# Kernel tuning notes

Hardware: AMD Instinct MI355X
Metric: run time of the kernel (lower is better)

The kernel has to match this reference:

```python
import jax, jax.numpy as jnp
import numpy as np

NUM_HEADS = 8
WINDOW = 7      # window_size -> K = 49 neighbors
DILATION = 1


def setup_inputs() -> dict:
    key = jax.random.key(0)
    k1, k2, k3 = jax.random.split(key, 3)
    shape = (4, 256, 48, 48)  # [B, C, H, W], C = num_heads * d_head
    return {
        "q": jax.random.normal(k1, shape, jnp.float32),
        "k": jax.random.normal(k2, shape, jnp.float32),
        "v": jax.random.normal(k3, shape, jnp.float32),
    }


def _neighbors(x, window, dilation):
    # x: [B, h, d, H, W] -> [B, h, K, d, H, W] via pad-and-slice shifts
    B, h, d, H, W = x.shape
    r = window // 2
    p = r * dilation
    xp = jnp.pad(x, ((0, 0), (0, 0), (0, 0), (p, p), (p, p)))
    offs = [(i - r) * dilation for i in range(window)]
    sl = [xp[:, :, :, p + dy:p + dy + H, p + dx:p + dx + W]
          for dy in offs for dx in offs]
    return jnp.stack(sl, axis=2)


def _valid_mask(H, W, window, dilation):
    # [K, H, W] boolean: True where the shifted neighbor is in-bounds
    r = window // 2
    offs = np.array([(i - r) * dilation for i in range(window)])
    hy = np.arange(H)[None, :] + offs[:, None]  # [window, H]
    wx = np.arange(W)[None, :] + offs[:, None]  # [window, W]
    vh = (hy >= 0) & (hy < H)
    vw = (wx >= 0) & (wx < W)
    mask = vh[:, None, :, None] & vw[None, :, None, :]  # [window, window, H, W]
    return jnp.asarray(mask.reshape(window * window, H, W))


def reference(q, k, v):
    B, C, H, W = q.shape
    h = NUM_HEADS
    d = C // h
    qh = q.reshape(B, h, d, H, W)
    kh = k.reshape(B, h, d, H, W)
    vh = v.reshape(B, h, d, H, W)
    kn = _neighbors(kh, WINDOW, DILATION)  # [B,h,K,d,H,W]
    vn = _neighbors(vh, WINDOW, DILATION)
    mask = _valid_mask(H, W, WINDOW, DILATION)[None, None]  # [1,1,K,H,W]
    scores = jnp.einsum('bhdxy,bhkdxy->bhkxy', qh, kn) * (d ** -0.5)
    scores = jnp.where(mask, scores, jnp.finfo(scores.dtype).min)
    attn = jax.nn.softmax(scores, axis=2)
    out = jnp.einsum('bhkxy,bhkdxy->bhdxy', attn, vn)
    return out.reshape(B, C, H, W)  # merge_heads
```

## Files before the change

### kernel.cpp

```cpp
#include <hip/hip_runtime.h>


#define H_IMG 48
#define W_IMG 48
#define DHEAD 32
#define NH    8
#define RAD   3
#define TW    16
#define TH    6
#define NWAVES TH
#define NTHREADS (64 * NWAVES)
#define HALO_W  (TW + 2*RAD)
#define HALO_H  (TH + 2*RAD)
#define HALO_PX (HALO_W * HALO_H)
#define KL_PX   (HALO_PX + 10)
#define KSTR    40
#define VROW    24
#define VSTR    (HALO_H * VROW + 8)
#define PSTR    40
#define PLANE   (H_IMG * W_IMG)

typedef _Float16 half_t;
typedef half_t half8_t __attribute__((ext_vector_type(8)));
typedef __fp16 fp16x2_t __attribute__((ext_vector_type(2)));
typedef float  f32x4  __attribute__((ext_vector_type(4)));

#if defined(__has_builtin)
#if __has_builtin(__builtin_amdgcn_exp2f)
#define EXP2F(x) __builtin_amdgcn_exp2f(x)
#endif
#endif
#ifndef EXP2F
#define EXP2F(x) __expf(0.6931471805599453f * (x))
#endif

__global__ __launch_bounds__(NTHREADS, 3)
void natten_f32_kernel(const float* __restrict__ q,
                       const float* __restrict__ k,
                       const float* __restrict__ v,
                       float* __restrict__ out) {
  __shared__ __align__(16) unsigned short kl[KL_PX * KSTR];
  __shared__ __align__(16) unsigned short vlT[DHEAD * VSTR];
  __shared__ __align__(16) unsigned short ps[NWAVES * 16 * PSTR];

  const int lane = threadIdx.x;
  const int wv   = threadIdx.y;
  const int tid  = lane + 64 * wv;
  const int c    = lane & 15;
  const int p    = lane >> 4;
  const int x0   = blockIdx.x * TW;
  const int y0   = blockIdx.y * TH;
  const size_t cbase = (size_t)blockIdx.z * DHEAD * PLANE;

  const int gqx = x0 + c;
  const int gqy = y0 + wv;

  const float S = 0.17677669529663687f * 1.4426950408889634f;
  const size_t qoff = cbase + (size_t)gqy * W_IMG + gqx;
  half8_t qf;
#pragma unroll
  for (int j = 0; j < 8; ++j)
    qf[j] = (half_t)(q[qoff + (size_t)(p * 8 + j) * PLANE] * S);

  float cm[2][4];
#pragma unroll
  for (int t = 0; t < 2; ++t)
#pragma unroll
    for (int r = 0; r < 4; ++r) {
      const int krel = t * 16 + 4 * p + r;
      const int gx = x0 + krel - RAD;
      cm[t][r] = ((unsigned)(krel - c) <= 6u &&
                  (unsigned)gx < (unsigned)W_IMG) ? 1.0f : 0.0f;
    }

  for (int i = tid; i < HALO_PX * 4; i += NTHREADS) {
    const int pix = i >> 2, chunk = i & 3;
    const int hy = pix / HALO_W;
    const int hx = pix - hy * HALO_W;
    int gy = y0 - RAD + hy;
    int gx = x0 - RAD + hx;
    gy = gy < 0 ? 0 : (gy > H_IMG - 1 ? H_IMG - 1 : gy);
    gx = gx < 0 ? 0 : (gx > W_IMG - 1 ? W_IMG - 1 : gx);
    const float* kb = k + cbase + (size_t)(chunk * 8) * PLANE + (size_t)gy * W_IMG + gx;
    union { half_t h[8]; uint4 u; } kk;
#pragma unroll
    for (int j = 0; j < 8; ++j) kk.h[j] = (half_t)kb[(size_t)j * PLANE];
    *(uint4*)&kl[pix * KSTR + chunk * 8] = kk.u;
  }
  if (tid < (KL_PX - HALO_PX) * (KSTR / 8)) {
    const uint4 z = make_uint4(0, 0, 0, 0);
    *(uint4*)&kl[HALO_PX * KSTR + tid * 8] = z;
  }

  for (int i = tid; i < DHEAD * HALO_H * 3; i += NTHREADS) {
    const int ch = i / (HALO_H * 3);
    const int rem = i - ch * (HALO_H * 3);
    const int row = rem / 3, oct = rem - row * 3;
    int gy = y0 - RAD + row;
    gy = gy < 0 ? 0 : (gy > H_IMG - 1 ? H_IMG - 1 : gy);
    const float* vb = v + cbase + (size_t)ch * PLANE + (size_t)gy * W_IMG;
    union { half_t h[8]; uint4 u; } vv;
#pragma unroll
    for (int j = 0; j < 8; ++j) {
      int s = oct * 8 + j;
      int hx = s > 21 ? 21 : s;
      int gx = x0 - RAD + hx;
      gx = gx < 0 ? 0 : (gx > W_IMG - 1 ? W_IMG - 1 : gx);
      vv.h[j] = (half_t)vb[gx];
    }
    *(uint4*)&vlT[ch * VSTR + row * VROW + oct * 8] = vv.u;
  }
  if (tid < DHEAD) {
    const uint4 z = make_uint4(0, 0, 0, 0);
    *(uint4*)&vlT[tid * VSTR + HALO_H * VROW] = z;
  }

  __syncthreads();

  f32x4 oa0 = {0.f, 0.f, 0.f, 0.f};
  f32x4 oa1 = {0.f, 0.f, 0.f, 0.f};
  const f32x4 z4 = {0.f, 0.f, 0.f, 0.f};
  float den = 0.0f;

  unsigned short* psq = &ps[(wv * 16 + c) * PSTR];

  for (int ry = 0; ry < 7; ++ry) {
    const int gy = gqy + ry - RAD;
    if ((unsigned)gy >= (unsigned)H_IMG) continue;
    const int hrow = wv + ry;

    union { uint4 u; half8_t h; } ka0, ka1, va0, va1, pb;
    ka0.u = *(const uint4*)&kl[(hrow * HALO_W + c) * KSTR + p * 8];
    ka1.u = *(const uint4*)&kl[(hrow * HALO_W + 16 + c) * KSTR + p * 8];
    va0.u = *(const uint4*)&vlT[c * VSTR + hrow * VROW + p * 8];
    va1.u = *(const uint4*)&vlT[(16 + c) * VSTR + hrow * VROW + p * 8];

    f32x4 s0 = __builtin_amdgcn_mfma_f32_16x16x32_f16(ka0.h, qf, z4, 0, 0, 0);
    f32x4 s1 = __builtin_amdgcn_mfma_f32_16x16x32_f16(ka1.h, qf, z4, 0, 0, 0);

    float pe0[4], pe1[4];
#pragma unroll
    for (int r = 0; r < 4; ++r) {
      pe0[r] = EXP2F(s0[r]) * cm[0][r];
      pe1[r] = EXP2F(s1[r]) * cm[1][r];
      den += pe0[r] + pe1[r];
    }
    union { fp16x2_t h[2]; uint2 u; } w0, w1;
    w0.h[0] = __builtin_amdgcn_cvt_pkrtz(pe0[0], pe0[1]);
    w0.h[1] = __builtin_amdgcn_cvt_pkrtz(pe0[2], pe0[3]);
    w1.h[0] = __builtin_amdgcn_cvt_pkrtz(pe1[0], pe1[1]);
    w1.h[1] = __builtin_amdgcn_cvt_pkrtz(pe1[2], pe1[3]);
    *(uint2*)((char*)psq + p * 8)      = w0.u;
    *(uint2*)((char*)psq + 32 + p * 8) = w1.u;

    pb.u = *(const uint4*)((const char*)psq + p * 16);

    oa0 = __builtin_amdgcn_mfma_f32_16x16x32_f16(va0.h, pb.h, oa0, 0, 0, 0);
    oa1 = __builtin_amdgcn_mfma_f32_16x16x32_f16(va1.h, pb.h, oa1, 0, 0, 0);
  }

  den += __shfl_xor(den, 16);
  den += __shfl_xor(den, 32);
  const float rden = 1.0f / den;

  const size_t obase = cbase + (size_t)gqy * W_IMG + x0 + c;
#pragma unroll
  for (int r = 0; r < 4; ++r) {
    out[obase + (size_t)(4 * p + r) * PLANE]      = oa0[r] * rden;
    out[obase + (size_t)(16 + 4 * p + r) * PLANE] = oa1[r] * rden;
  }
}

extern "C" void kernel_launch(void* const* d_in, const int* in_sizes, int n_in,
                              void* d_out, int out_size, void* d_ws, size_t ws_size,
                              hipStream_t stream) {
  const float* q = (const float*)d_in[0];
  const float* k = (const float*)d_in[1];
  const float* v = (const float*)d_in[2];
  float* out = (float*)d_out;

  dim3 grid(W_IMG / TW, H_IMG / TH, 4 * NH);
  dim3 block(64, NWAVES, 1);
  hipLaunchKernelGGL(natten_f32_kernel, grid, block, 0, stream, q, k, v, out);
}
```

Before: 96.49 us.

## Feed softmax weights directly from registers into 16x16x16 MFMAs, drop LDS staging

The P·V product now uses two 16x16x16 MFMAs per output tile, which take the softmax weights straight from the register layout the score MFMA produces, so the per-iteration LDS store/load round trip through the ps buffer goes away. Out-of-image rows are no longer skipped with a branch. Instead they get a large negative bias through the MFMA accumulator input, and the loop is fully unrolled. Launch bounds are raised to allow more resident blocks. In exchange, each tile issues twice as many smaller MFMAs, the boundary rows do wasted work, and tighter register limits may cause spills.

Result: no change. 94.78 us (-1.8%).

```diff
diff --git a/kernel.cpp b/kernel.cpp
--- a/kernel.cpp
+++ b/kernel.cpp
@@ -17,10 +17,10 @@
 #define KSTR    40
 #define VROW    24
 #define VSTR    (HALO_H * VROW + 8)
-#define PSTR    40
 #define PLANE   (H_IMG * W_IMG)
 
 typedef _Float16 half_t;
+typedef half_t half4_t __attribute__((ext_vector_type(4)));
 typedef half_t half8_t __attribute__((ext_vector_type(8)));
 typedef __fp16 fp16x2_t __attribute__((ext_vector_type(2)));
 typedef float  f32x4  __attribute__((ext_vector_type(4)));
@@ -34,14 +34,13 @@
 #define EXP2F(x) __expf(0.6931471805599453f * (x))
 #endif
 
-__global__ __launch_bounds__(NTHREADS, 3)
+__global__ __launch_bounds__(NTHREADS, 5)
 void natten_f32_kernel(const float* __restrict__ q,
                        const float* __restrict__ k,
                        const float* __restrict__ v,
                        float* __restrict__ out) {
   __shared__ __align__(16) unsigned short kl[KL_PX * KSTR];
   __shared__ __align__(16) unsigned short vlT[DHEAD * VSTR];
-  __shared__ __align__(16) unsigned short ps[NWAVES * 16 * PSTR];
 
   const int lane = threadIdx.x;
   const int wv   = threadIdx.y;
@@ -119,24 +118,32 @@
 
   f32x4 oa0 = {0.f, 0.f, 0.f, 0.f};
   f32x4 oa1 = {0.f, 0.f, 0.f, 0.f};
-  const f32x4 z4 = {0.f, 0.f, 0.f, 0.f};
   float den = 0.0f;
 
-  unsigned short* psq = &ps[(wv * 16 + c) * PSTR];
+  const unsigned short* klrow  = &kl[c * KSTR + p * 8];
+  const unsigned short* klrow1 = &kl[(16 + c) * KSTR + p * 8];
+  const unsigned short* v0row  = &vlT[c * VSTR + 4 * p];
+  const unsigned short* v1row  = &vlT[(16 + c) * VSTR + 4 * p];
 
+#pragma unroll
   for (int ry = 0; ry < 7; ++ry) {
+    const int hrow = wv + ry;
     const int gy = gqy + ry - RAD;
-    if ((unsigned)gy >= (unsigned)H_IMG) continue;
-    const int hrow = wv + ry;
+    const float bias = ((unsigned)gy < (unsigned)H_IMG) ? 0.0f : -16384.0f;
+    const f32x4 ci = {bias, bias, bias, bias};
 
-    union { uint4 u; half8_t h; } ka0, ka1, va0, va1, pb;
-    ka0.u = *(const uint4*)&kl[(hrow * HALO_W + c) * KSTR + p * 8];
-    ka1.u = *(const uint4*)&kl[(hrow * HALO_W + 16 + c) * KSTR + p * 8];
-    va0.u = *(const uint4*)&vlT[c * VSTR + hrow * VROW + p * 8];
-    va1.u = *(const uint4*)&vlT[(16 + c) * VSTR + hrow * VROW + p * 8];
+    union { uint4 u; half8_t h; } ka0, ka1;
+    ka0.u = *(const uint4*)(klrow  + hrow * (HALO_W * KSTR));
+    ka1.u = *(const uint4*)(klrow1 + hrow * (HALO_W * KSTR));
 
-    f32x4 s0 = __builtin_amdgcn_mfma_f32_16x16x32_f16(ka0.h, qf, z4, 0, 0, 0);
-    f32x4 s1 = __builtin_amdgcn_mfma_f32_16x16x32_f16(ka1.h, qf, z4, 0, 0, 0);
+    union { uint2 u; half4_t h; } va00, va01, va10, va11;
+    va00.u = *(const uint2*)(v0row + hrow * VROW);
+    va01.u = *(const uint2*)(v0row + hrow * VROW + 16);
+    va10.u = *(const uint2*)(v1row + hrow * VROW);
+    va11.u = *(const uint2*)(v1row + hrow * VROW + 16);
+
+    f32x4 s0 = __builtin_amdgcn_mfma_f32_16x16x32_f16(ka0.h, qf, ci, 0, 0, 0);
+    f32x4 s1 = __builtin_amdgcn_mfma_f32_16x16x32_f16(ka1.h, qf, ci, 0, 0, 0);
 
     float pe0[4], pe1[4];
 #pragma unroll
@@ -145,18 +152,16 @@
       pe1[r] = EXP2F(s1[r]) * cm[1][r];
       den += pe0[r] + pe1[r];
     }
-    union { fp16x2_t h[2]; uint2 u; } w0, w1;
-    w0.h[0] = __builtin_amdgcn_cvt_pkrtz(pe0[0], pe0[1]);
-    w0.h[1] = __builtin_amdgcn_cvt_pkrtz(pe0[2], pe0[3]);
-    w1.h[0] = __builtin_amdgcn_cvt_pkrtz(pe1[0], pe1[1]);
-    w1.h[1] = __builtin_amdgcn_cvt_pkrtz(pe1[2], pe1[3]);
-    *(uint2*)((char*)psq + p * 8)      = w0.u;
-    *(uint2*)((char*)psq + 32 + p * 8) = w1.u;
+    union { fp16x2_t h2[2]; half4_t h4; } w0, w1;
+    w0.h2[0] = __builtin_amdgcn_cvt_pkrtz(pe0[0], pe0[1]);
+    w0.h2[1] = __builtin_amdgcn_cvt_pkrtz(pe0[2], pe0[3]);
+    w1.h2[0] = __builtin_amdgcn_cvt_pkrtz(pe1[0], pe1[1]);
+    w1.h2[1] = __builtin_amdgcn_cvt_pkrtz(pe1[2], pe1[3]);
 
-    pb.u = *(const uint4*)((const char*)psq + p * 16);
-
-    oa0 = __builtin_amdgcn_mfma_f32_16x16x32_f16(va0.h, pb.h, oa0, 0, 0, 0);
-    oa1 = __builtin_amdgcn_mfma_f32_16x16x32_f16(va1.h, pb.h, oa1, 0, 0, 0);
+    oa0 = __builtin_amdgcn_mfma_f32_16x16x16f16(va00.h, w0.h4, oa0, 0, 0, 0);
+    oa0 = __builtin_amdgcn_mfma_f32_16x16x16f16(va01.h, w1.h4, oa0, 0, 0, 0);
+    oa1 = __builtin_amdgcn_mfma_f32_16x16x16f16(va10.h, w0.h4, oa1, 0, 0, 0);
+    oa1 = __builtin_amdgcn_mfma_f32_16x16x16f16(va11.h, w1.h4, oa1, 0, 0, 0);
   }
 
   den += __shfl_xor(den, 16);
```
